# Performance work log

Hardware: AMD Instinct MI355X
Metric: run time of the kernel (lower is better)

Reference implementation:

```python
import jax, jax.numpy as jnp
import numpy as np

B, S, D, H, E, K = 4, 2048, 1024, 4096, 8, 2


def setup_inputs() -> dict:
    key = jax.random.key(0)
    ks = jax.random.split(key, 7)
    sd = 1.0 / np.sqrt(D)
    sh = 1.0 / np.sqrt(H)
    return {
        "x": jax.random.normal(ks[0], (B, S, D), dtype=jnp.float32),
        "Wg": jax.random.uniform(ks[1], (D, E), jnp.float32, -sd, sd),
        "bg": jnp.zeros((E,), jnp.float32),
        "W1": jax.random.uniform(ks[2], (E, D, H), jnp.float32, -sd, sd),
        "b1": jax.random.uniform(ks[3], (E, H), jnp.float32, -sd, sd),
        "W2": jax.random.uniform(ks[4], (E, H, D), jnp.float32, -sh, sh),
        "b2": jax.random.uniform(ks[5], (E, D), jnp.float32, -sh, sh),
    }


def reference(x, Wg, bg, W1, b1, W2, b2):
    # gating: softmax over experts, then top-k
    probs = jax.nn.softmax(x @ Wg + bg, axis=-1)            # [B,S,E]
    topv, topi = jax.lax.top_k(probs, K)                     # [B,S,K]
    # NOTE: original computes normalized scores but uses RAW top-k scores
    # scatter raw top-k scores back to dense per-expert weights [B,S,E]
    onehot = jax.nn.one_hot(topi, E, dtype=x.dtype)          # [B,S,K,E]
    w_dense = jnp.einsum("bske,bsk->bse", onehot, topv)      # [B,S,E]
    out = jnp.zeros_like(x)
    for e in range(E):
        h = jax.nn.relu(jnp.einsum("bsd,dh->bsh", x, W1[e]) + b1[e])
        y = jnp.einsum("bsh,hd->bsd", h, W2[e]) + b2[e]
        out = out + y * w_dense[..., e:e + 1]
    return out
```

## Files before the change

### kernel.cpp

```cpp
#include <hip/hip_runtime.h>

typedef unsigned short u16;
typedef __attribute__((ext_vector_type(8))) short bf16x8;
typedef __attribute__((ext_vector_type(8))) unsigned short u16x8;
typedef __attribute__((ext_vector_type(4))) float f32x4;

#define NTOK 8192
#define DDIM 1024
#define HDIM 4096
#define NEXP 8

typedef __attribute__((address_space(1))) const void gvoid;
typedef __attribute__((address_space(3))) void lvoid;

__device__ __forceinline__ u16 f2b(float f) {
  unsigned u = __float_as_uint(f);
  u += 0x7fffu + ((u >> 16) & 1u);
  return (u16)(u >> 16);
}
__device__ __forceinline__ void glds16(const void* g, void* l) {
  __builtin_amdgcn_global_load_lds((gvoid*)g, (lvoid*)l, 16, 0, 0);
}

__global__ void convert_x_kernel(const float* __restrict__ src, u16* __restrict__ dst) {
  size_t i = ((size_t)blockIdx.x * 256 + threadIdx.x) * 8;
  float4 a = *(const float4*)(src + i);
  float4 b = *(const float4*)(src + i + 4);
  u16x8 o;
  o[0] = f2b(a.x); o[1] = f2b(a.y); o[2] = f2b(a.z); o[3] = f2b(a.w);
  o[4] = f2b(b.x); o[5] = f2b(b.y); o[6] = f2b(b.z); o[7] = f2b(b.w);
  *(u16x8*)(dst + i) = o;
}

__global__ void transpose_kernel(const float* __restrict__ src, u16* __restrict__ dst,
                                 int R, int C) {
  int e = blockIdx.z;
  src += (size_t)e * R * C;
  dst += (size_t)e * R * C;
  int r0 = blockIdx.y * 64, c0 = blockIdx.x * 64;
  __shared__ u16 T[64][68];
  int t = threadIdx.x;
  int rr = t >> 4, cc = (t & 15) * 4;
#pragma unroll
  for (int i = 0; i < 4; ++i) {
    int r = i * 16 + rr;
    float4 v = *(const float4*)(src + (size_t)(r0 + r) * C + c0 + cc);
    T[cc + 0][r] = f2b(v.x);
    T[cc + 1][r] = f2b(v.y);
    T[cc + 2][r] = f2b(v.z);
    T[cc + 3][r] = f2b(v.w);
  }
  __syncthreads();
#pragma unroll
  for (int i = 0; i < 4; ++i) {
    int c = i * 16 + rr;
    ushort4 o = *(const ushort4*)&T[c][cc];
    *(ushort4*)(dst + (size_t)(c0 + c) * R + r0 + cc) = o;
  }
}

__global__ void gate_kernel(const float* __restrict__ x, const float* __restrict__ Wg,
                            const float* __restrict__ bg, int* __restrict__ counts,
                            int* __restrict__ pair_tok, float* __restrict__ pair_w,
                            int* __restrict__ tok_ep)
{
  int lane = threadIdx.x & 63;
  int wave = threadIdx.x >> 6;
  int tok = blockIdx.x * 4 + wave;
  const float* xr = x + (size_t)tok * DDIM + lane * 16;
  float acc[NEXP];
#pragma unroll
  for (int e = 0; e < NEXP; ++e) acc[e] = 0.f;
#pragma unroll
  for (int j = 0; j < 16; ++j) {
    float xf = xr[j];
    const float* wr = Wg + (size_t)(lane * 16 + j) * NEXP;
    float4 wa = *(const float4*)(wr);
    float4 wb = *(const float4*)(wr + 4);
    acc[0] = fmaf(xf, wa.x, acc[0]);
    acc[1] = fmaf(xf, wa.y, acc[1]);
    acc[2] = fmaf(xf, wa.z, acc[2]);
    acc[3] = fmaf(xf, wa.w, acc[3]);
    acc[4] = fmaf(xf, wb.x, acc[4]);
    acc[5] = fmaf(xf, wb.y, acc[5]);
    acc[6] = fmaf(xf, wb.z, acc[6]);
    acc[7] = fmaf(xf, wb.w, acc[7]);
  }
#pragma unroll
  for (int off = 32; off > 0; off >>= 1) {
#pragma unroll
    for (int e = 0; e < NEXP; ++e) acc[e] += __shfl_xor(acc[e], off, 64);
  }
  if (lane == 0) {
    float l[NEXP];
    float mx = -3.4e38f;
#pragma unroll
    for (int e = 0; e < NEXP; ++e) { l[e] = acc[e] + bg[e]; mx = fmaxf(mx, l[e]); }
    float s = 0.f;
#pragma unroll
    for (int e = 0; e < NEXP; ++e) { l[e] = __expf(l[e] - mx); s += l[e]; }
    float inv = 1.f / s;
    float v1 = -1.f; int i1 = 0;
#pragma unroll
    for (int e = 0; e < NEXP; ++e) { if (l[e] > v1) { v1 = l[e]; i1 = e; } }
    float v2 = -1.f; int i2 = 0;
#pragma unroll
    for (int e = 0; e < NEXP; ++e) { if (e != i1 && l[e] > v2) { v2 = l[e]; i2 = e; } }
    int p1 = atomicAdd(&counts[i1], 1);
    pair_tok[i1 * NTOK + p1] = tok;
    pair_w[i1 * NTOK + p1] = v1 * inv;
    int p2 = atomicAdd(&counts[i2], 1);
    pair_tok[i2 * NTOK + p2] = tok;
    pair_w[i2 * NTOK + p2] = v2 * inv;
    tok_ep[2 * tok + 0] = (i1 << 16) | p1;
    tok_ep[2 * tok + 1] = (i2 << 16) | p2;
  }
}

__global__ void offsets_kernel(const int* __restrict__ counts, int* __restrict__ offsets) {
  if (threadIdx.x == 0) {
    int s = 0;
    for (int e = 0; e < NEXP; ++e) { offsets[e] = s; s += counts[e]; }
  }
}

__device__ __forceinline__ void stage4(const u16* xa0, const u16* xa1,
                                       const u16* wb0, const u16* wb1,
                                       u16* Asb, u16* Bsb, int wave, int koff) {
  glds16(xa0 + koff, Asb + wave * 512);
  glds16(xa1 + koff, Asb + 2048 + wave * 512);
  glds16(wb0 + koff, Bsb + wave * 512);
  glds16(wb1 + koff, Bsb + 2048 + wave * 512);
}

__device__ __forceinline__ void mfma_tile(const u16* Asb, const u16* Bsb,
                                          f32x4 (&acc)[4][4],
                                          int wrr, int wc, int ln, int q) {
  bf16x8 af[4], bfr[4];
#pragma unroll
  for (int mt = 0; mt < 4; ++mt)
    af[mt] = *(const bf16x8*)(Asb + (wrr + mt * 16 + ln) * 32 + q * 8);
#pragma unroll
  for (int nt = 0; nt < 4; ++nt)
    bfr[nt] = *(const bf16x8*)(Bsb + (wc + nt * 16 + ln) * 32 + q * 8);
#pragma unroll
  for (int mt = 0; mt < 4; ++mt)
#pragma unroll
    for (int nt = 0; nt < 4; ++nt)
      acc[mt][nt] = __builtin_amdgcn_mfma_f32_16x16x32_bf16(af[mt], bfr[nt], acc[mt][nt], 0, 0, 0);
}

__global__ __launch_bounds__(256) void gemm1_kernel(
    const u16* __restrict__ xb, const u16* __restrict__ W1T,
    const float* __restrict__ b1, const int* __restrict__ counts,
    const int* __restrict__ offsets, const int* __restrict__ pair_tok,
    u16* __restrict__ h, int hp, int p0)
{
  int e = blockIdx.y;
  int cnt = counts[e];
  int i0 = blockIdx.z * 128;
  if (i0 >= cnt) return;
  int n0 = blockIdx.x * 128;

  __shared__ __align__(16) u16 As[2][128 * 32];
  __shared__ __align__(16) u16 Bs[2][128 * 32];

  int t = threadIdx.x;
  int lane = t & 63;
  int wave = t >> 6;
  int rlim = cnt - i0;

  const int* tokp = pair_tok + e * NTOK + i0;
  int arow = t >> 2;
  int c8 = (t & 3) * 8;
  const u16* xa0 = xb + (size_t)tokp[min(arow, rlim - 1)] * DDIM + c8;
  const u16* xa1 = xb + (size_t)tokp[min(arow + 64, rlim - 1)] * DDIM + c8;
  const u16* wb0 = W1T + (size_t)e * HDIM * DDIM + (size_t)(p0 + n0 + arow) * DDIM + c8;
  const u16* wb1 = wb0 + (size_t)64 * DDIM;

  f32x4 acc[4][4] = {};
  int wrr = (wave >> 1) * 64;
  int wc = (wave & 1) * 64;
  int ln = lane & 15;
  int q = lane >> 4;

  stage4(xa0, xa1, wb0, wb1, As[0], Bs[0], wave, 0);
  __syncthreads();
  for (int k0 = 0; k0 < DDIM; k0 += 64) {
    stage4(xa0, xa1, wb0, wb1, As[1], Bs[1], wave, k0 + 32);
    __builtin_amdgcn_sched_barrier(0);
    mfma_tile(As[0], Bs[0], acc, wrr, wc, ln, q);
    __syncthreads();
    if (k0 + 64 < DDIM) {
      stage4(xa0, xa1, wb0, wb1, As[0], Bs[0], wave, k0 + 64);
      __builtin_amdgcn_sched_barrier(0);
    }
    mfma_tile(As[1], Bs[1], acc, wrr, wc, ln, q);
    __syncthreads();
  }

  int ob = offsets[e];
  float bb[4];
#pragma unroll
  for (int nt = 0; nt < 4; ++nt)
    bb[nt] = b1[(size_t)e * HDIM + p0 + n0 + wc + nt * 16 + ln];
  size_t hbase = (size_t)(ob + i0) * hp + n0 + wc;
#pragma unroll
  for (int mt = 0; mt < 4; ++mt) {
#pragma unroll
    for (int r = 0; r < 4; ++r) {
      int row = wrr + mt * 16 + q * 4 + r;
      if (row < rlim) {
        u16* hrow = h + hbase + (size_t)row * hp;
#pragma unroll
        for (int nt = 0; nt < 4; ++nt) {
          float v = acc[mt][nt][r] + bb[nt];
          hrow[nt * 16 + ln] = f2b(fmaxf(v, 0.f));
        }
      }
    }
  }
}

__global__ __launch_bounds__(256) void gemm2_kernel(
    const u16* __restrict__ h, const u16* __restrict__ W2T,
    const float* __restrict__ b2v, const int* __restrict__ counts,
    const int* __restrict__ offsets, float* __restrict__ y,
    int hp, int p0, int first)
{
  int e = blockIdx.x;
  int cnt = counts[e];
  int i0 = blockIdx.z * 128;
  if (i0 >= cnt) return;
  int n0 = blockIdx.y * 128;

  __shared__ __align__(16) u16 As[2][128 * 32];
  __shared__ __align__(16) u16 Bs[2][128 * 32];

  int t = threadIdx.x;
  int lane = t & 63;
  int wave = t >> 6;
  int rlim = cnt - i0;
  int rbase = offsets[e] + i0;

  int arow = t >> 2;
  int c8 = (t & 3) * 8;
  const u16* xa0 = h + (size_t)(rbase + arow) * hp + c8;
  const u16* xa1 = h + (size_t)(rbase + arow + 64) * hp + c8;
  const u16* wb0 = W2T + (size_t)e * DDIM * HDIM + (size_t)(n0 + arow) * HDIM + p0 + c8;
  const u16* wb1 = wb0 + (size_t)64 * HDIM;

  f32x4 acc[4][4] = {};
  int wrr = (wave >> 1) * 64;
  int wc = (wave & 1) * 64;
  int ln = lane & 15;
  int q = lane >> 4;

  stage4(xa0, xa1, wb0, wb1, As[0], Bs[0], wave, 0);
  __syncthreads();
  for (int k0 = 0; k0 < hp; k0 += 64) {
    stage4(xa0, xa1, wb0, wb1, As[1], Bs[1], wave, k0 + 32);
    __builtin_amdgcn_sched_barrier(0);
    mfma_tile(As[0], Bs[0], acc, wrr, wc, ln, q);
    __syncthreads();
    if (k0 + 64 < hp) {
      stage4(xa0, xa1, wb0, wb1, As[0], Bs[0], wave, k0 + 64);
      __builtin_amdgcn_sched_barrier(0);
    }
    mfma_tile(As[1], Bs[1], acc, wrr, wc, ln, q);
    __syncthreads();
  }

  float bb[4];
#pragma unroll
  for (int nt = 0; nt < 4; ++nt)
    bb[nt] = first ? b2v[(size_t)e * DDIM + n0 + wc + nt * 16 + ln] : 0.f;
#pragma unroll
  for (int mt = 0; mt < 4; ++mt) {
#pragma unroll
    for (int r = 0; r < 4; ++r) {
      int row = wrr + mt * 16 + q * 4 + r;
      if (row < rlim) {
        float* yr = y + (size_t)(rbase + row) * DDIM + n0 + wc;
#pragma unroll
        for (int nt = 0; nt < 4; ++nt) {
          float v = acc[mt][nt][r] + bb[nt];
          if (first) yr[nt * 16 + ln] = v;
          else       yr[nt * 16 + ln] += v;
        }
      }
    }
  }
}

__global__ __launch_bounds__(256) void combine_kernel(
    const float* __restrict__ y, const int* __restrict__ tok_ep,
    const float* __restrict__ pair_w, const int* __restrict__ offsets,
    float* __restrict__ out)
{
  int tok = blockIdx.x;
  int ep1 = tok_ep[2 * tok + 0];
  int ep2 = tok_ep[2 * tok + 1];
  int e1 = ep1 >> 16, p1 = ep1 & 0xffff;
  int e2 = ep2 >> 16, p2 = ep2 & 0xffff;
  float w1 = pair_w[e1 * NTOK + p1];
  float w2 = pair_w[e2 * NTOK + p2];
  const float* r1 = y + (size_t)(offsets[e1] + p1) * DDIM;
  const float* r2 = y + (size_t)(offsets[e2] + p2) * DDIM;
  int c = threadIdx.x * 4;
  float4 a = *(const float4*)(r1 + c);
  float4 b = *(const float4*)(r2 + c);
  float4 o;
  o.x = w1 * a.x + w2 * b.x;
  o.y = w1 * a.y + w2 * b.y;
  o.z = w1 * a.z + w2 * b.z;
  o.w = w1 * a.w + w2 * b.w;
  *(float4*)(out + (size_t)tok * DDIM + c) = o;
}

extern "C" void kernel_launch(void* const* d_in, const int* in_sizes, int n_in,
                              void* d_out, int out_size, void* d_ws, size_t ws_size,
                              hipStream_t stream)
{
  const float* x  = (const float*)d_in[0];
  const float* Wg = (const float*)d_in[1];
  const float* bg = (const float*)d_in[2];
  const float* W1 = (const float*)d_in[3];
  const float* b1 = (const float*)d_in[4];
  const float* W2 = (const float*)d_in[5];
  const float* b2 = (const float*)d_in[6];
  float* out = (float*)d_out;

  char* ws = (char*)d_ws;
  int*   counts   = (int*)(ws + 0);
  int*   offsets  = (int*)(ws + 64);
  int*   tok_ep   = (int*)(ws + 128);
  int*   pair_tok = (int*)(ws + 128 + 65536);
  float* pair_w   = (float*)(ws + 128 + 65536 + 262144);
  u16*   xb  = (u16*)(ws + 589952);
  u16*   W1T = (u16*)(ws + 589952 + 16777216);
  u16*   W2T = (u16*)(ws + 589952 + 16777216 + 67108864);
  float* yb  = (float*)(ws + 589952 + 16777216 + 2 * (size_t)67108864);
  u16*   hbuf = (u16*)(ws + 589952 + 16777216 + 3 * (size_t)67108864);
  size_t used_base = 589952 + 16777216 + 3 * (size_t)67108864;

  int hp = 128;
  const int cands[6] = {4096, 2048, 1024, 512, 256, 128};
  for (int ci = 0; ci < 6; ++ci) {
    if (used_base + (size_t)16512 * cands[ci] * 2 <= ws_size) { hp = cands[ci]; break; }
  }

  hipMemsetAsync(counts, 0, 64, stream);
  convert_x_kernel<<<NTOK * DDIM / 2048, 256, 0, stream>>>(x, xb);
  transpose_kernel<<<dim3(HDIM / 64, DDIM / 64, NEXP), 256, 0, stream>>>(W1, W1T, DDIM, HDIM);
  transpose_kernel<<<dim3(DDIM / 64, HDIM / 64, NEXP), 256, 0, stream>>>(W2, W2T, HDIM, DDIM);
  gate_kernel<<<NTOK / 4, 256, 0, stream>>>(x, Wg, bg, counts, pair_tok, pair_w, tok_ep);
  offsets_kernel<<<1, 64, 0, stream>>>(counts, offsets);
  for (int p0 = 0; p0 < HDIM; p0 += hp) {
    gemm1_kernel<<<dim3(hp / 128, NEXP, 64), 256, 0, stream>>>(
        xb, W1T, b1, counts, offsets, pair_tok, hbuf, hp, p0);
    gemm2_kernel<<<dim3(NEXP, DDIM / 128, 64), 256, 0, stream>>>(
        hbuf, W2T, b2, counts, offsets, yb, hp, p0, p0 == 0 ? 1 : 0);
  }
  combine_kernel<<<NTOK, 256, 0, stream>>>(yb, tok_ep, pair_w, offsets, out);
}
```

Before: 963.7 us.

## Use 256x256 GEMM tiles with 8 waves, swizzled LDS and phased prefetch

Both expert GEMMs move from 128x128 tiles with 4 waves and K-step 32 to 256x256 tiles with 8 waves, K-step 64 and 128 KB of dynamic LDS. Operands are stored in an XOR-swizzled LDS layout to avoid bank conflicts. The main loop interleaves async global-to-LDS loads across four MFMA phases with barriers and s_setprio. The goal is more operand reuse per byte loaded and better overlap of loads with MFMA work. The trade-offs are higher register pressure (32 accumulators per wave), fewer blocks per CU, and more wasted work on partial expert tiles.

```diff
diff --git a/kernel.cpp b/kernel.cpp
--- a/kernel.cpp
+++ b/kernel.cpp
@@ -124,105 +124,151 @@
   }
 }
 
-__device__ __forceinline__ void stage4(const u16* xa0, const u16* xa1,
-                                       const u16* wb0, const u16* wb1,
-                                       u16* Asb, u16* Bsb, int wave, int koff) {
-  glds16(xa0 + koff, Asb + wave * 512);
-  glds16(xa1 + koff, Asb + 2048 + wave * 512);
-  glds16(wb0 + koff, Bsb + wave * 512);
-  glds16(wb1 + koff, Bsb + 2048 + wave * 512);
-}
-
-__device__ __forceinline__ void mfma_tile(const u16* Asb, const u16* Bsb,
-                                          f32x4 (&acc)[4][4],
-                                          int wrr, int wc, int ln, int q) {
-  bf16x8 af[4], bfr[4];
-#pragma unroll
-  for (int mt = 0; mt < 4; ++mt)
-    af[mt] = *(const bf16x8*)(Asb + (wrr + mt * 16 + ln) * 32 + q * 8);
-#pragma unroll
-  for (int nt = 0; nt < 4; ++nt)
-    bfr[nt] = *(const bf16x8*)(Bsb + (wc + nt * 16 + ln) * 32 + q * 8);
-#pragma unroll
-  for (int mt = 0; mt < 4; ++mt)
-#pragma unroll
-    for (int nt = 0; nt < 4; ++nt)
-      acc[mt][nt] = __builtin_amdgcn_mfma_f32_16x16x32_bf16(af[mt], bfr[nt], acc[mt][nt], 0, 0, 0);
-}
-
-__global__ __launch_bounds__(256) void gemm1_kernel(
+#define MFMA16 __builtin_amdgcn_mfma_f32_16x16x32_bf16
+
+#define MM2(mt, A0, A1) \
+  acc[mt][0] = MFMA16(A0, b00, acc[mt][0], 0, 0, 0); \
+  acc[mt][1] = MFMA16(A0, b10, acc[mt][1], 0, 0, 0); \
+  acc[mt][2] = MFMA16(A0, b20, acc[mt][2], 0, 0, 0); \
+  acc[mt][3] = MFMA16(A0, b30, acc[mt][3], 0, 0, 0); \
+  acc[mt][0] = MFMA16(A1, b01, acc[mt][0], 0, 0, 0); \
+  acc[mt][1] = MFMA16(A1, b11, acc[mt][1], 0, 0, 0); \
+  acc[mt][2] = MFMA16(A1, b21, acc[mt][2], 0, 0, 0); \
+  acc[mt][3] = MFMA16(A1, b31, acc[mt][3], 0, 0, 0)
+
+#define DSA(mt, ks) (*(const bf16x8*)(Ab + (mt) * 2048 + ((ks) ? qs1 : qs0)))
+#define DSB(nt, ks) (*(const bf16x8*)(Bb + (nt) * 2048 + ((ks) ? qs1 : qs0)))
+
+#define BARM() do { __builtin_amdgcn_s_barrier(); asm volatile("" ::: "memory"); } while (0)
+#define PH_SYNC() do { __builtin_amdgcn_s_barrier();                        \
+  asm volatile("s_waitcnt lgkmcnt(0)" ::: "memory");                        \
+  __builtin_amdgcn_sched_barrier(0); } while (0)
+
+#define GEMM_MAINLOOP(NK)                                                    \
+  glds16(pA00, dA00); glds16(pA01, dA01);                                    \
+  glds16(pA10, dA10); glds16(pA11, dA11);                                    \
+  glds16(pB00, dB00); glds16(pB01, dB01);                                    \
+  glds16(pB10, dB10); glds16(pB11, dB11);                                    \
+  glds16(pA00 + 64, dA00 + 16384); glds16(pA01 + 64, dA01 + 16384);          \
+  asm volatile("s_waitcnt vmcnt(2)" ::: "memory");                           \
+  BARM();                                                                    \
+  for (int k = 0; k < (NK); ++k) {                                           \
+    int cur = k & 1, nxt = cur ^ 1;                                          \
+    const char* Ab = ldsc + cur * 32768 + abase;                             \
+    const char* Bb = ldsc + 65536 + cur * 32768 + bbase;                     \
+    int kk = (k + 1) * 64;                                                   \
+    bool pf = (k + 1 < (NK));                                                \
+    if (pf) { glds16(pA10 + kk, dA10 + nxt * 16384);                         \
+              glds16(pA11 + kk, dA11 + nxt * 16384); }                       \
+    bf16x8 b00 = DSB(0, 0), b01 = DSB(0, 1), b10 = DSB(1, 0), b11 = DSB(1, 1);\
+    bf16x8 b20 = DSB(2, 0), b21 = DSB(2, 1), b30 = DSB(3, 0), b31 = DSB(3, 1);\
+    bf16x8 a0 = DSA(0, 0), a1 = DSA(0, 1), a2 = DSA(1, 0), a3 = DSA(1, 1);   \
+    PH_SYNC();                                                               \
+    __builtin_amdgcn_s_setprio(1); MM2(0, a0, a1); MM2(1, a2, a3);           \
+    __builtin_amdgcn_s_setprio(0); BARM();                                   \
+    if (pf) { glds16(pB00 + kk, dB00 + nxt * 16384);                         \
+              glds16(pB01 + kk, dB01 + nxt * 16384); }                       \
+    a0 = DSA(2, 0); a1 = DSA(2, 1); a2 = DSA(3, 0); a3 = DSA(3, 1);          \
+    PH_SYNC();                                                               \
+    __builtin_amdgcn_s_setprio(1); MM2(2, a0, a1); MM2(3, a2, a3);           \
+    __builtin_amdgcn_s_setprio(0); BARM();                                   \
+    if (pf) { glds16(pB10 + kk, dB10 + nxt * 16384);                         \
+              glds16(pB11 + kk, dB11 + nxt * 16384); }                       \
+    a0 = DSA(4, 0); a1 = DSA(4, 1); a2 = DSA(5, 0); a3 = DSA(5, 1);          \
+    PH_SYNC();                                                               \
+    __builtin_amdgcn_s_setprio(1); MM2(4, a0, a1); MM2(5, a2, a3);           \
+    __builtin_amdgcn_s_setprio(0); BARM();                                   \
+    a0 = DSA(6, 0); a1 = DSA(6, 1); a2 = DSA(7, 0); a3 = DSA(7, 1);          \
+    PH_SYNC();                                                               \
+    __builtin_amdgcn_s_setprio(1); MM2(6, a0, a1); MM2(7, a2, a3);           \
+    __builtin_amdgcn_s_setprio(0); BARM();                                   \
+    if (k + 2 < (NK)) {                                                      \
+      glds16(pA00 + kk + 64, dA00 + cur * 16384);                            \
+      glds16(pA01 + kk + 64, dA01 + cur * 16384);                            \
+      asm volatile("s_waitcnt vmcnt(2)" ::: "memory");                       \
+      BARM();                                                                \
+    } else if (pf) {                                                         \
+      asm volatile("s_waitcnt vmcnt(0)" ::: "memory");                       \
+      BARM();                                                                \
+    }                                                                        \
+  }
+
+#define STAGE_MAP()                                                          \
+  int t = threadIdx.x;                                                       \
+  int wv = t >> 6;                                                           \
+  int lane = t & 63;                                                         \
+  int ln = lane & 15, q = lane >> 4;                                         \
+  int wm = wv >> 2, wn = wv & 3;                                             \
+  int o0 = t * 16, o1 = 8192 + t * 16;                                       \
+  int r0 = o0 >> 7, r1 = o1 >> 7;                                            \
+  int c0 = ((o0 ^ (((o0 >> 7) & 7) << 4)) & 127) >> 1;                       \
+  int c1 = ((o1 ^ (((o1 >> 7) & 7) << 4)) & 127) >> 1;                       \
+  int sw = (ln & 7) << 4;                                                    \
+  int qs0 = (q * 16) ^ sw;                                                   \
+  int qs1 = (64 + q * 16) ^ sw;                                              \
+  int abase = wm * 16384 + ln * 128;                                         \
+  int bbase = (wn >> 1) * 16384 + (wn & 1) * 8192 + ln * 128;                \
+  u16* dA00 = lds_u16 + wv * 512;                                            \
+  u16* dA01 = lds_u16 + 4096 + wv * 512;                                     \
+  u16* dA10 = lds_u16 + 8192 + wv * 512;                                     \
+  u16* dA11 = lds_u16 + 12288 + wv * 512;                                    \
+  u16* dB00 = lds_u16 + 32768 + wv * 512;                                    \
+  u16* dB01 = lds_u16 + 32768 + 4096 + wv * 512;                             \
+  u16* dB10 = lds_u16 + 32768 + 8192 + wv * 512;                             \
+  u16* dB11 = lds_u16 + 32768 + 12288 + wv * 512;                            \
+  const char* ldsc = (const char*)lds_u16;
+
+__global__ __launch_bounds__(512, 2) void gemm1_kernel(
     const u16* __restrict__ xb, const u16* __restrict__ W1T,
     const float* __restrict__ b1, const int* __restrict__ counts,
     const int* __restrict__ offsets, const int* __restrict__ pair_tok,
     u16* __restrict__ h, int hp, int p0)
 {
-  int e = blockIdx.y;
+  int e = blockIdx.x;
   int cnt = counts[e];
-  int i0 = blockIdx.z * 128;
+  int i0 = blockIdx.z * 256;
   if (i0 >= cnt) return;
-  int n0 = blockIdx.x * 128;
-
-  __shared__ __align__(16) u16 As[2][128 * 32];
-  __shared__ __align__(16) u16 Bs[2][128 * 32];
-
-  int t = threadIdx.x;
-  int lane = t & 63;
-  int wave = t >> 6;
+  int n0 = blockIdx.y * 256;
+  extern __shared__ u16 lds_u16[];
+
+  STAGE_MAP();
   int rlim = cnt - i0;
-
+  int rl = rlim - 1;
   const int* tokp = pair_tok + e * NTOK + i0;
-  int arow = t >> 2;
-  int c8 = (t & 3) * 8;
-  const u16* xa0 = xb + (size_t)tokp[min(arow, rlim - 1)] * DDIM + c8;
-  const u16* xa1 = xb + (size_t)tokp[min(arow + 64, rlim - 1)] * DDIM + c8;
-  const u16* wb0 = W1T + (size_t)e * HDIM * DDIM + (size_t)(p0 + n0 + arow) * DDIM + c8;
-  const u16* wb1 = wb0 + (size_t)64 * DDIM;
-
-  f32x4 acc[4][4] = {};
-  int wrr = (wave >> 1) * 64;
-  int wc = (wave & 1) * 64;
-  int ln = lane & 15;
-  int q = lane >> 4;
-
-  stage4(xa0, xa1, wb0, wb1, As[0], Bs[0], wave, 0);
-  __syncthreads();
-  for (int k0 = 0; k0 < DDIM; k0 += 64) {
-    stage4(xa0, xa1, wb0, wb1, As[1], Bs[1], wave, k0 + 32);
-    __builtin_amdgcn_sched_barrier(0);
-    mfma_tile(As[0], Bs[0], acc, wrr, wc, ln, q);
-    __syncthreads();
-    if (k0 + 64 < DDIM) {
-      stage4(xa0, xa1, wb0, wb1, As[0], Bs[0], wave, k0 + 64);
-      __builtin_amdgcn_sched_barrier(0);
-    }
-    mfma_tile(As[1], Bs[1], acc, wrr, wc, ln, q);
-    __syncthreads();
-  }
+  const u16* pA00 = xb + (size_t)tokp[min(r0, rl)] * DDIM + c0;
+  const u16* pA01 = xb + (size_t)tokp[min(r1, rl)] * DDIM + c1;
+  const u16* pA10 = xb + (size_t)tokp[min(128 + r0, rl)] * DDIM + c0;
+  const u16* pA11 = xb + (size_t)tokp[min(128 + r1, rl)] * DDIM + c1;
+  const u16* wbb = W1T + (size_t)e * HDIM * DDIM + (size_t)(p0 + n0) * DDIM;
+  const u16* pB00 = wbb + (size_t)r0 * DDIM + c0;
+  const u16* pB01 = wbb + (size_t)r1 * DDIM + c1;
+  const u16* pB10 = wbb + (size_t)(128 + r0) * DDIM + c0;
+  const u16* pB11 = wbb + (size_t)(128 + r1) * DDIM + c1;
+
+  f32x4 acc[8][4] = {};
+  GEMM_MAINLOOP(DDIM / 64);
 
   int ob = offsets[e];
   float bb[4];
 #pragma unroll
   for (int nt = 0; nt < 4; ++nt)
-    bb[nt] = b1[(size_t)e * HDIM + p0 + n0 + wc + nt * 16 + ln];
-  size_t hbase = (size_t)(ob + i0) * hp + n0 + wc;
-#pragma unroll
-  for (int mt = 0; mt < 4; ++mt) {
-#pragma unroll
-    for (int r = 0; r < 4; ++r) {
-      int row = wrr + mt * 16 + q * 4 + r;
+    bb[nt] = b1[(size_t)e * HDIM + p0 + n0 + wn * 64 + nt * 16 + ln];
+#pragma unroll
+  for (int mt = 0; mt < 8; ++mt) {
+#pragma unroll
+    for (int rr = 0; rr < 4; ++rr) {
+      int row = wm * 128 + mt * 16 + q * 4 + rr;
       if (row < rlim) {
-        u16* hrow = h + hbase + (size_t)row * hp;
-#pragma unroll
-        for (int nt = 0; nt < 4; ++nt) {
-          float v = acc[mt][nt][r] + bb[nt];
-          hrow[nt * 16 + ln] = f2b(fmaxf(v, 0.f));
-        }
+        u16* hrow = h + (size_t)(ob + i0 + row) * hp + n0 + wn * 64;
+#pragma unroll
+        for (int nt = 0; nt < 4; ++nt)
+          hrow[nt * 16 + ln] = f2b(fmaxf(acc[mt][nt][rr] + bb[nt], 0.f));
       }
     }
   }
 }
 
-__global__ __launch_bounds__(256) void gemm2_kernel(
+__global__ __launch_bounds__(512, 2) void gemm2_kernel(
     const u16* __restrict__ h, const u16* __restrict__ W2T,
     const float* __restrict__ b2v, const int* __restrict__ counts,
     const int* __restrict__ offsets, float* __restrict__ y,
@@ -230,61 +276,43 @@
 {
   int e = blockIdx.x;
   int cnt = counts[e];
-  int i0 = blockIdx.z * 128;
+  int i0 = blockIdx.z * 256;
   if (i0 >= cnt) return;
-  int n0 = blockIdx.y * 128;
-
-  __shared__ __align__(16) u16 As[2][128 * 32];
-  __shared__ __align__(16) u16 Bs[2][128 * 32];
-
-  int t = threadIdx.x;
-  int lane = t & 63;
-  int wave = t >> 6;
+  int n0 = blockIdx.y * 256;
+  extern __shared__ u16 lds_u16[];
+
+  STAGE_MAP();
   int rlim = cnt - i0;
+  int rl = rlim - 1;
   int rbase = offsets[e] + i0;
-
-  int arow = t >> 2;
-  int c8 = (t & 3) * 8;
-  const u16* xa0 = h + (size_t)(rbase + arow) * hp + c8;
-  const u16* xa1 = h + (size_t)(rbase + arow + 64) * hp + c8;
-  const u16* wb0 = W2T + (size_t)e * DDIM * HDIM + (size_t)(n0 + arow) * HDIM + p0 + c8;
-  const u16* wb1 = wb0 + (size_t)64 * HDIM;
-
-  f32x4 acc[4][4] = {};
-  int wrr = (wave >> 1) * 64;
-  int wc = (wave & 1) * 64;
-  int ln = lane & 15;
-  int q = lane >> 4;
-
-  stage4(xa0, xa1, wb0, wb1, As[0], Bs[0], wave, 0);
-  __syncthreads();
-  for (int k0 = 0; k0 < hp; k0 += 64) {
-    stage4(xa0, xa1, wb0, wb1, As[1], Bs[1], wave, k0 + 32);
-    __builtin_amdgcn_sched_barrier(0);
-    mfma_tile(As[0], Bs[0], acc, wrr, wc, ln, q);
-    __syncthreads();
-    if (k0 + 64 < hp) {
-      stage4(xa0, xa1, wb0, wb1, As[0], Bs[0], wave, k0 + 64);
-      __builtin_amdgcn_sched_barrier(0);
-    }
-    mfma_tile(As[1], Bs[1], acc, wrr, wc, ln, q);
-    __syncthreads();
-  }
+  const u16* pA00 = h + (size_t)(rbase + min(r0, rl)) * hp + c0;
+  const u16* pA01 = h + (size_t)(rbase + min(r1, rl)) * hp + c1;
+  const u16* pA10 = h + (size_t)(rbase + min(128 + r0, rl)) * hp + c0;
+  const u16* pA11 = h + (size_t)(rbase + min(128 + r1, rl)) * hp + c1;
+  const u16* wbb = W2T + (size_t)e * DDIM * HDIM + (size_t)n0 * HDIM + p0;
+  const u16* pB00 = wbb + (size_t)r0 * HDIM + c0;
+  const u16* pB01 = wbb + (size_t)r1 * HDIM + c1;
+  const u16* pB10 = wbb + (size_t)(128 + r0) * HDIM + c0;
+  const u16* pB11 = wbb + (size_t)(128 + r1) * HDIM + c1;
+
+  f32x4 acc[8][4] = {};
+  int nk = hp >> 6;
+  GEMM_MAINLOOP(nk);
 
   float bb[4];
 #pragma unroll
   for (int nt = 0; nt < 4; ++nt)
-    bb[nt] = first ? b2v[(size_t)e * DDIM + n0 + wc + nt * 16 + ln] : 0.f;
-#pragma unroll
-  for (int mt = 0; mt < 4; ++mt) {
-#pragma unroll
-    for (int r = 0; r < 4; ++r) {
-      int row = wrr + mt * 16 + q * 4 + r;
+    bb[nt] = first ? b2v[(size_t)e * DDIM + n0 + wn * 64 + nt * 16 + ln] : 0.f;
+#pragma unroll
+  for (int mt = 0; mt < 8; ++mt) {
+#pragma unroll
+    for (int rr = 0; rr < 4; ++rr) {
+      int row = wm * 128 + mt * 16 + q * 4 + rr;
       if (row < rlim) {
-        float* yr = y + (size_t)(rbase + row) * DDIM + n0 + wc;
+        float* yr = y + (size_t)(rbase + row) * DDIM + n0 + wn * 64;
 #pragma unroll
         for (int nt = 0; nt < 4; ++nt) {
-          float v = acc[mt][nt][r] + bb[nt];
+          float v = acc[mt][nt][rr] + bb[nt];
           if (first) yr[nt * 16 + ln] = v;
           else       yr[nt * 16 + ln] += v;
         }
@@ -344,11 +372,16 @@
   u16*   hbuf = (u16*)(ws + 589952 + 16777216 + 3 * (size_t)67108864);
   size_t used_base = 589952 + 16777216 + 3 * (size_t)67108864;
 
-  int hp = 128;
-  const int cands[6] = {4096, 2048, 1024, 512, 256, 128};
-  for (int ci = 0; ci < 6; ++ci) {
+  int hp = 256;
+  const int cands[5] = {4096, 2048, 1024, 512, 256};
+  for (int ci = 0; ci < 5; ++ci) {
     if (used_base + (size_t)16512 * cands[ci] * 2 <= ws_size) { hp = cands[ci]; break; }
   }
+
+  hipFuncSetAttribute((const void*)gemm1_kernel,
+                      hipFuncAttributeMaxDynamicSharedMemorySize, 131072);
+  hipFuncSetAttribute((const void*)gemm2_kernel,
+                      hipFuncAttributeMaxDynamicSharedMemorySize, 131072);
 
   hipMemsetAsync(counts, 0, 64, stream);
   convert_x_kernel<<<NTOK * DDIM / 2048, 256, 0, stream>>>(x, xb);
@@ -357,9 +390,9 @@
   gate_kernel<<<NTOK / 4, 256, 0, stream>>>(x, Wg, bg, counts, pair_tok, pair_w, tok_ep);
   offsets_kernel<<<1, 64, 0, stream>>>(counts, offsets);
   for (int p0 = 0; p0 < HDIM; p0 += hp) {
-    gemm1_kernel<<<dim3(hp / 128, NEXP, 64), 256, 0, stream>>>(
+    gemm1_kernel<<<dim3(NEXP, hp / 256, 32), 512, 131072, stream>>>(
         xb, W1T, b1, counts, offsets, pair_tok, hbuf, hp, p0);
-    gemm2_kernel<<<dim3(NEXP, DDIM / 128, 64), 256, 0, stream>>>(
+    gemm2_kernel<<<dim3(NEXP, DDIM / 256, 32), 512, 131072, stream>>>(
         hbuf, W2T, b2, counts, offsets, yb, hp, p0, p0 == 0 ? 1 : 0);
   }
   combine_kernel<<<NTOK, 256, 0, stream>>>(yb, tok_ep, pair_w, offsets, out);
```

After: 943.7 us. -2.1%, faster.

## Use compact expert tile list for grouped GEMMs and pad atomic counters

Applied to the files above, without the earlier changes.

The gate kernel now increments per-expert counters spaced 128 bytes apart, so concurrent atomics from different experts do not land on the same cache line. The offsets kernel builds a compact list of (expert, row-tile) pairs, and both GEMM kernels launch over that list with the tile index in blockIdx.x. This replaces the dense 8x64 grid, where most blocks exited early, and changes the block ordering so consecutive blocks share the same weight column tile. It also clamps A-row reads in gemm2, drops the hp=128 chunk size, and adds a small serial tile-list build plus extra indirection loads per block.

```diff
diff --git a/kernel.cpp b/kernel.cpp
--- a/kernel.cpp
+++ b/kernel.cpp
@@ -60,7 +60,7 @@
 }
 
 __global__ void gate_kernel(const float* __restrict__ x, const float* __restrict__ Wg,
-                            const float* __restrict__ bg, int* __restrict__ counts,
+                            const float* __restrict__ bg, int* __restrict__ counts_pad,
                             int* __restrict__ pair_tok, float* __restrict__ pair_w,
                             int* __restrict__ tok_ep)
 {
@@ -106,21 +106,31 @@
     float v2 = -1.f; int i2 = 0;
 #pragma unroll
     for (int e = 0; e < NEXP; ++e) { if (e != i1 && l[e] > v2) { v2 = l[e]; i2 = e; } }
-    int p1 = atomicAdd(&counts[i1], 1);
+    int p1 = atomicAdd(&counts_pad[i1 * 32], 1);
     pair_tok[i1 * NTOK + p1] = tok;
     pair_w[i1 * NTOK + p1] = v1 * inv;
-    int p2 = atomicAdd(&counts[i2], 1);
+    tok_ep[2 * tok + 0] = (i1 << 16) | p1;
+    int p2 = atomicAdd(&counts_pad[i2 * 32], 1);
     pair_tok[i2 * NTOK + p2] = tok;
     pair_w[i2 * NTOK + p2] = v2 * inv;
-    tok_ep[2 * tok + 0] = (i1 << 16) | p1;
     tok_ep[2 * tok + 1] = (i2 << 16) | p2;
   }
 }
 
-__global__ void offsets_kernel(const int* __restrict__ counts, int* __restrict__ offsets) {
+__global__ void offsets_kernel(const int* __restrict__ counts_pad, int* __restrict__ counts,
+                               int* __restrict__ offsets, int* __restrict__ tile_e,
+                               int* __restrict__ tile_i0, int* __restrict__ ntiles)
+{
   if (threadIdx.x == 0) {
     int s = 0;
-    for (int e = 0; e < NEXP; ++e) { offsets[e] = s; s += counts[e]; }
+    for (int e = 0; e < NEXP; ++e) {
+      int c = counts_pad[e * 32];
+      counts[e] = c; offsets[e] = s; s += c;
+    }
+    int nt_ = 0;
+    for (int e = 0; e < NEXP; ++e)
+      for (int i0 = 0; i0 < counts[e]; i0 += 128) { tile_e[nt_] = e; tile_i0[nt_] = i0; nt_++; }
+    *ntiles = nt_;
   }
 }
 
@@ -153,14 +163,16 @@
 __global__ __launch_bounds__(256) void gemm1_kernel(
     const u16* __restrict__ xb, const u16* __restrict__ W1T,
     const float* __restrict__ b1, const int* __restrict__ counts,
-    const int* __restrict__ offsets, const int* __restrict__ pair_tok,
-    u16* __restrict__ h, int hp, int p0)
-{
-  int e = blockIdx.y;
+    const int* __restrict__ offsets, const int* __restrict__ ntiles,
+    const int* __restrict__ tile_e, const int* __restrict__ tile_i0,
+    const int* __restrict__ pair_tok, u16* __restrict__ h, int hp, int p0)
+{
+  int bx = blockIdx.x;
+  if (bx >= *ntiles) return;
+  int e = tile_e[bx];
+  int i0 = tile_i0[bx];
   int cnt = counts[e];
-  int i0 = blockIdx.z * 128;
-  if (i0 >= cnt) return;
-  int n0 = blockIdx.x * 128;
+  int n0 = blockIdx.y * 128;
 
   __shared__ __align__(16) u16 As[2][128 * 32];
   __shared__ __align__(16) u16 Bs[2][128 * 32];
@@ -169,12 +181,13 @@
   int lane = t & 63;
   int wave = t >> 6;
   int rlim = cnt - i0;
+  int rl = rlim - 1;
 
   const int* tokp = pair_tok + e * NTOK + i0;
   int arow = t >> 2;
   int c8 = (t & 3) * 8;
-  const u16* xa0 = xb + (size_t)tokp[min(arow, rlim - 1)] * DDIM + c8;
-  const u16* xa1 = xb + (size_t)tokp[min(arow + 64, rlim - 1)] * DDIM + c8;
+  const u16* xa0 = xb + (size_t)tokp[min(arow, rl)] * DDIM + c8;
+  const u16* xa1 = xb + (size_t)tokp[min(arow + 64, rl)] * DDIM + c8;
   const u16* wb0 = W1T + (size_t)e * HDIM * DDIM + (size_t)(p0 + n0 + arow) * DDIM + c8;
   const u16* wb1 = wb0 + (size_t)64 * DDIM;
 
@@ -225,13 +238,15 @@
 __global__ __launch_bounds__(256) void gemm2_kernel(
     const u16* __restrict__ h, const u16* __restrict__ W2T,
     const float* __restrict__ b2v, const int* __restrict__ counts,
-    const int* __restrict__ offsets, float* __restrict__ y,
-    int hp, int p0, int first)
-{
-  int e = blockIdx.x;
+    const int* __restrict__ offsets, const int* __restrict__ ntiles,
+    const int* __restrict__ tile_e, const int* __restrict__ tile_i0,
+    float* __restrict__ y, int hp, int p0, int first)
+{
+  int bx = blockIdx.x;
+  if (bx >= *ntiles) return;
+  int e = tile_e[bx];
+  int i0 = tile_i0[bx];
   int cnt = counts[e];
-  int i0 = blockIdx.z * 128;
-  if (i0 >= cnt) return;
   int n0 = blockIdx.y * 128;
 
   __shared__ __align__(16) u16 As[2][128 * 32];
@@ -241,12 +256,13 @@
   int lane = t & 63;
   int wave = t >> 6;
   int rlim = cnt - i0;
+  int rl = rlim - 1;
   int rbase = offsets[e] + i0;
 
   int arow = t >> 2;
   int c8 = (t & 3) * 8;
-  const u16* xa0 = h + (size_t)(rbase + arow) * hp + c8;
-  const u16* xa1 = h + (size_t)(rbase + arow + 64) * hp + c8;
+  const u16* xa0 = h + (size_t)(rbase + min(arow, rl)) * hp + c8;
+  const u16* xa1 = h + (size_t)(rbase + min(arow + 64, rl)) * hp + c8;
   const u16* wb0 = W2T + (size_t)e * DDIM * HDIM + (size_t)(n0 + arow) * HDIM + p0 + c8;
   const u16* wb1 = wb0 + (size_t)64 * HDIM;
 
@@ -332,35 +348,39 @@
   float* out = (float*)d_out;
 
   char* ws = (char*)d_ws;
-  int*   counts   = (int*)(ws + 0);
-  int*   offsets  = (int*)(ws + 64);
-  int*   tok_ep   = (int*)(ws + 128);
-  int*   pair_tok = (int*)(ws + 128 + 65536);
-  float* pair_w   = (float*)(ws + 128 + 65536 + 262144);
-  u16*   xb  = (u16*)(ws + 589952);
-  u16*   W1T = (u16*)(ws + 589952 + 16777216);
-  u16*   W2T = (u16*)(ws + 589952 + 16777216 + 67108864);
-  float* yb  = (float*)(ws + 589952 + 16777216 + 2 * (size_t)67108864);
-  u16*   hbuf = (u16*)(ws + 589952 + 16777216 + 3 * (size_t)67108864);
-  size_t used_base = 589952 + 16777216 + 3 * (size_t)67108864;
-
-  int hp = 128;
-  const int cands[6] = {4096, 2048, 1024, 512, 256, 128};
-  for (int ci = 0; ci < 6; ++ci) {
+  int*   counts_pad = (int*)(ws + 0);
+  int*   counts     = (int*)(ws + 1024);
+  int*   offsets    = (int*)(ws + 1056);
+  int*   ntiles     = (int*)(ws + 1088);
+  int*   tile_e     = (int*)(ws + 1152);
+  int*   tile_i0    = (int*)(ws + 2176);
+  int*   tok_ep     = (int*)(ws + 4096);
+  int*   pair_tok   = (int*)(ws + 69632);
+  float* pair_w     = (float*)(ws + 331776);
+  u16*   xb  = (u16*)(ws + 593920);
+  u16*   W1T = (u16*)(ws + 593920 + 16777216);
+  u16*   W2T = (u16*)(ws + 593920 + 16777216 + 67108864);
+  float* yb  = (float*)(ws + 593920 + 16777216 + 2 * (size_t)67108864);
+  u16*   hbuf = (u16*)(ws + 593920 + 16777216 + 3 * (size_t)67108864);
+  size_t used_base = 593920 + 16777216 + 3 * (size_t)67108864;
+
+  int hp = 256;
+  const int cands[5] = {4096, 2048, 1024, 512, 256};
+  for (int ci = 0; ci < 5; ++ci) {
     if (used_base + (size_t)16512 * cands[ci] * 2 <= ws_size) { hp = cands[ci]; break; }
   }
 
-  hipMemsetAsync(counts, 0, 64, stream);
+  hipMemsetAsync(counts_pad, 0, 1024, stream);
   convert_x_kernel<<<NTOK * DDIM / 2048, 256, 0, stream>>>(x, xb);
   transpose_kernel<<<dim3(HDIM / 64, DDIM / 64, NEXP), 256, 0, stream>>>(W1, W1T, DDIM, HDIM);
   transpose_kernel<<<dim3(DDIM / 64, HDIM / 64, NEXP), 256, 0, stream>>>(W2, W2T, HDIM, DDIM);
-  gate_kernel<<<NTOK / 4, 256, 0, stream>>>(x, Wg, bg, counts, pair_tok, pair_w, tok_ep);
-  offsets_kernel<<<1, 64, 0, stream>>>(counts, offsets);
+  gate_kernel<<<NTOK / 4, 256, 0, stream>>>(x, Wg, bg, counts_pad, pair_tok, pair_w, tok_ep);
+  offsets_kernel<<<1, 64, 0, stream>>>(counts_pad, counts, offsets, tile_e, tile_i0, ntiles);
   for (int p0 = 0; p0 < HDIM; p0 += hp) {
-    gemm1_kernel<<<dim3(hp / 128, NEXP, 64), 256, 0, stream>>>(
-        xb, W1T, b1, counts, offsets, pair_tok, hbuf, hp, p0);
-    gemm2_kernel<<<dim3(NEXP, DDIM / 128, 64), 256, 0, stream>>>(
-        hbuf, W2T, b2, counts, offsets, yb, hp, p0, p0 == 0 ? 1 : 0);
+    gemm1_kernel<<<dim3(136, hp / 128), 256, 0, stream>>>(
+        xb, W1T, b1, counts, offsets, ntiles, tile_e, tile_i0, pair_tok, hbuf, hp, p0);
+    gemm2_kernel<<<dim3(136, DDIM / 128), 256, 0, stream>>>(
+        hbuf, W2T, b2, counts, offsets, ntiles, tile_e, tile_i0, yb, hp, p0, p0 == 0 ? 1 : 0);
   }
   combine_kernel<<<NTOK, 256, 0, stream>>>(yb, tok_ep, pair_w, offsets, out);
 }
```

Result: faster. 839.2 us (-12.9%).
